# Performance work log

Hardware: AMD Instinct MI355X
Metric: run time of the kernel (lower is better)

Reference implementation:

```python
import jax, jax.numpy as jnp
import numpy as np

N_NODES = 100000  # m == n for the square adjacency
LEAKY_SLOPE = 0.5


def setup_inputs() -> dict:
    key = jax.random.key(0)
    k1, k2, k3 = jax.random.split(key, 3)
    E = 3200000
    D = 128
    edge_index = jax.random.randint(k1, (2, E), 0, N_NODES, dtype=jnp.int64)
    edge_vals = jax.random.uniform(k2, (E,), dtype=jnp.float32)
    embeds = jax.random.normal(k3, (N_NODES, D), dtype=jnp.float32)
    return {"edge_index": edge_index, "edge_vals": edge_vals, "embeds": embeds}


def reference(edge_index, edge_vals, embeds):
    # coalesce (sum duplicate (row,col) values) followed by scatter-add SpMM
    # is equivalent to scatter-add SpMM directly on un-coalesced indices.
    row, col = edge_index[0], edge_index[1]
    # gather source embeddings, scale by edge values, segment-sum into rows
    msgs = edge_vals[:, None] * embeds[col]                 # [E, D]
    agg = jax.ops.segment_sum(msgs, row, num_segments=N_NODES)  # [N, D]
    return jax.nn.leaky_relu(agg, negative_slope=LEAKY_SLOPE)
```

## Files before the change

kernel.cpp:

```cpp
#include <hip/hip_runtime.h>
#include <hip/hip_fp16.h>


#define GCN_D       128
#define LEAKY_SLOPE 0.5f
#define NBLK        256
#define RPB         64
#define RPB_SH      6
#define CAP         3072
#define NBINS_MAX   2048
#define SCAN_G      512
#define NCHAIN_FB   4

typedef float    f32x2 __attribute__((ext_vector_type(2)));
typedef float    f32x4 __attribute__((ext_vector_type(4)));
typedef unsigned u32x2 __attribute__((ext_vector_type(2)));
typedef unsigned u32x4 __attribute__((ext_vector_type(4)));

__device__ inline unsigned pack_half2(float a, float b) {
    __half2 h = __floats2half2_rn(a, b);
    return *reinterpret_cast<unsigned*>(&h);
}


__global__ void hist_convert_kernel(const int* __restrict__ row,
                                    int E, int CH, int nbins,
                                    unsigned* __restrict__ hist,
                                    const f32x4* __restrict__ emb4,
                                    int n8,
                                    u32x4* __restrict__ h8) {
    __shared__ unsigned h[NBINS_MAX];
    if ((int)blockIdx.x < NBLK) {
        int b = blockIdx.x;
        for (int i = threadIdx.x; i < nbins; i += blockDim.x) h[i] = 0u;
        __syncthreads();
        int s = b * CH;
        int e = min(E, s + CH);
        for (int i = s + threadIdx.x; i < e; i += blockDim.x)
            atomicAdd(&h[row[i] >> RPB_SH], 1u);
        __syncthreads();
        for (int i = threadIdx.x; i < nbins; i += blockDim.x)
            hist[(long long)i * NBLK + b] = h[i];
    } else {
        int bid = (int)blockIdx.x - NBLK;
        int nb  = (int)gridDim.x - NBLK;
        int stride = nb * blockDim.x;
        for (int i = bid * blockDim.x + threadIdx.x; i < n8; i += stride) {
            f32x4 a  = __builtin_nontemporal_load(&emb4[2 * i]);
            f32x4 b2 = __builtin_nontemporal_load(&emb4[2 * i + 1]);
            u32x4 o;
            o.x = pack_half2(a.x, a.y);
            o.y = pack_half2(a.z, a.w);
            o.z = pack_half2(b2.x, b2.y);
            o.w = pack_half2(b2.z, b2.w);
            h8[i] = o;
        }
    }
}


__global__ void __launch_bounds__(256)
scanA_kernel(const unsigned* __restrict__ data, int M, int chunk,
             unsigned* __restrict__ bsum) {
    __shared__ unsigned red[256];
    int b = blockIdx.x, t = threadIdx.x;
    long long s = (long long)b * chunk;
    unsigned acc = 0;
    for (int i = t; i < chunk; i += 256) {
        long long j = s + i;
        if (j < M) acc += data[j];
    }
    red[t] = acc;
    __syncthreads();
    for (int off = 128; off > 0; off >>= 1) {
        if (t < off) red[t] += red[t + off];
        __syncthreads();
    }
    if (t == 0) bsum[b] = red[0];
}

__global__ void __launch_bounds__(512)
scanB_kernel(unsigned* __restrict__ bsum, int G) {
    __shared__ unsigned s[512];
    int t = threadIdx.x;
    unsigned v = (t < G) ? bsum[t] : 0u;
    s[t] = v;
    __syncthreads();
    for (int off = 1; off < 512; off <<= 1) {
        unsigned u = (t >= off) ? s[t - off] : 0u;
        __syncthreads();
        s[t] += u;
        __syncthreads();
    }
    if (t < G) bsum[t] = (t == 0) ? 0u : s[t - 1];
}

__global__ void __launch_bounds__(256)
scanC_kernel(unsigned* __restrict__ data, int M, int chunk,
             const unsigned* __restrict__ bsum) {
    __shared__ unsigned pre[256];
    int b = blockIdx.x, t = threadIdx.x;
    long long s0 = (long long)b * chunk;
    long long s1 = s0 + chunk;
    int ept = (chunk + 255) / 256;
    long long ts = s0 + (long long)t * ept;

    unsigned acc = 0;
    for (int i = 0; i < ept; ++i) {
        long long j = ts + i;
        if (j < s1 && j < M) acc += data[j];
    }
    pre[t] = acc;
    __syncthreads();
    for (int off = 1; off < 256; off <<= 1) {
        unsigned u = (t >= off) ? pre[t - off] : 0u;
        __syncthreads();
        pre[t] += u;
        __syncthreads();
    }
    unsigned run = bsum[b] + ((t == 0) ? 0u : pre[t - 1]);
    for (int i = 0; i < ept; ++i) {
        long long j = ts + i;
        if (j < s1 && j < M) {
            unsigned v = data[j];
            data[j] = run;
            run += v;
        }
    }
}


__global__ void scatter_kernel(const int* __restrict__ row,
                               const int* __restrict__ col,
                               const float* __restrict__ val,
                               int E, int CH, int nbins,
                               const unsigned* __restrict__ scanned,
                               u32x2* __restrict__ entry) {
    __shared__ unsigned cur[NBINS_MAX];
    int b = blockIdx.x;
    for (int i = threadIdx.x; i < nbins; i += blockDim.x)
        cur[i] = scanned[(long long)i * NBLK + b];
    __syncthreads();

    int s = b * CH;
    int e = min(E, s + CH);
    for (int i = s + threadIdx.x; i < e; i += blockDim.x) {
        int r = row[i];
        unsigned key = ((unsigned)(r & (RPB - 1)) << 17) | (unsigned)col[i];
        unsigned pos = atomicAdd(&cur[r >> RPB_SH], 1u);
        u32x2 q; q.x = key; q.y = __float_as_uint(val[i]);
        entry[pos] = q;
    }
}


__global__ void __launch_bounds__(512)
bin_reduce_kernel(const unsigned* __restrict__ scanned,
                  const u32x2* __restrict__ entry,
                  const __half2* __restrict__ ebh,
                  float* __restrict__ out,
                  int E, int N, int nbins) {
    __shared__ u32x2    sorted[CAP];
    __shared__ unsigned cnt[RPB];
    __shared__ unsigned offs[RPB];
    __shared__ unsigned cur[RPB];

    int b    = blockIdx.x;
    int tid  = threadIdx.x;
    int wave = tid >> 6;
    int lane = tid & 63;

    int seg0 = (int)scanned[(long long)b * NBLK];
    int seg1 = (b + 1 < nbins) ? (int)scanned[(long long)(b + 1) * NBLK] : E;

    float ax[8], ay[8];
    #pragma unroll
    for (int j = 0; j < 8; ++j) { ax[j] = 0.f; ay[j] = 0.f; }

    for (int cs = seg0; cs < seg1; cs += CAP) {
        int n = min(CAP, seg1 - cs);

        if (tid < RPB) cnt[tid] = 0u;
        __syncthreads();

        for (int i = tid; i < n; i += 512) {
            u32x2 q = __builtin_nontemporal_load(&entry[cs + i]);
            atomicAdd(&cnt[q.x >> 17], 1u);
        }
        __syncthreads();

        if (tid == 0) {
            unsigned run = 0;
            for (int r = 0; r < RPB; ++r) {
                offs[r] = run; cur[r] = run; run += cnt[r];
            }
        }
        __syncthreads();

        for (int i = tid; i < n; i += 512) {
            u32x2 q = __builtin_nontemporal_load(&entry[cs + i]);
            unsigned pos = atomicAdd(&cur[q.x >> 17], 1u);
            sorted[pos] = q;
        }
        __syncthreads();

        #pragma unroll
        for (int j = 0; j < 8; ++j) {
            int r  = (wave << 3) + j;
            int s  = (int)offs[r];
            int en = s + (int)cnt[r];
            int i  = s;
            for (; i + 8 <= en; i += 8) {
                u32x2 q0 = sorted[i],     q1 = sorted[i + 1];
                u32x2 q2 = sorted[i + 2], q3 = sorted[i + 3];
                u32x2 q4 = sorted[i + 4], q5 = sorted[i + 5];
                u32x2 q6 = sorted[i + 6], q7 = sorted[i + 7];
                __half2 m0 = ebh[(long long)(q0.x & 0x1FFFFu) * 64 + lane];
                __half2 m1 = ebh[(long long)(q1.x & 0x1FFFFu) * 64 + lane];
                __half2 m2 = ebh[(long long)(q2.x & 0x1FFFFu) * 64 + lane];
                __half2 m3 = ebh[(long long)(q3.x & 0x1FFFFu) * 64 + lane];
                __half2 m4 = ebh[(long long)(q4.x & 0x1FFFFu) * 64 + lane];
                __half2 m5 = ebh[(long long)(q5.x & 0x1FFFFu) * 64 + lane];
                __half2 m6 = ebh[(long long)(q6.x & 0x1FFFFu) * 64 + lane];
                __half2 m7 = ebh[(long long)(q7.x & 0x1FFFFu) * 64 + lane];
                float2 f;
                f = __half22float2(m0);
                ax[j] += __uint_as_float(q0.y) * f.x; ay[j] += __uint_as_float(q0.y) * f.y;
                f = __half22float2(m1);
                ax[j] += __uint_as_float(q1.y) * f.x; ay[j] += __uint_as_float(q1.y) * f.y;
                f = __half22float2(m2);
                ax[j] += __uint_as_float(q2.y) * f.x; ay[j] += __uint_as_float(q2.y) * f.y;
                f = __half22float2(m3);
                ax[j] += __uint_as_float(q3.y) * f.x; ay[j] += __uint_as_float(q3.y) * f.y;
                f = __half22float2(m4);
                ax[j] += __uint_as_float(q4.y) * f.x; ay[j] += __uint_as_float(q4.y) * f.y;
                f = __half22float2(m5);
                ax[j] += __uint_as_float(q5.y) * f.x; ay[j] += __uint_as_float(q5.y) * f.y;
                f = __half22float2(m6);
                ax[j] += __uint_as_float(q6.y) * f.x; ay[j] += __uint_as_float(q6.y) * f.y;
                f = __half22float2(m7);
                ax[j] += __uint_as_float(q7.y) * f.x; ay[j] += __uint_as_float(q7.y) * f.y;
            }
            for (; i < en; ++i) {
                u32x2 q = sorted[i];
                __half2 mm = ebh[(long long)(q.x & 0x1FFFFu) * 64 + lane];
                float2 f = __half22float2(mm);
                ax[j] += __uint_as_float(q.y) * f.x;
                ay[j] += __uint_as_float(q.y) * f.y;
            }
        }
        __syncthreads();
    }

    int gr0 = b * RPB + (wave << 3);
    #pragma unroll
    for (int j = 0; j < 8; ++j) {
        int gr = gr0 + j;
        if (gr < N) {
            float x = ax[j], y = ay[j];
            x = x > 0.f ? x : LEAKY_SLOPE * x;
            y = y > 0.f ? y : LEAKY_SLOPE * y;
            f32x2 o; o.x = x; o.y = y;
            __builtin_nontemporal_store(
                o, reinterpret_cast<f32x2*>(out) + (long long)gr * 64 + lane);
        }
    }
}


__global__ void build_nodes_kernel(const int* __restrict__ row,
                                   const int* __restrict__ col,
                                   const float* __restrict__ val,
                                   int E,
                                   int* __restrict__ head,
                                   int4* __restrict__ node) {
    int stride = gridDim.x * blockDim.x;
    for (int i = blockIdx.x * blockDim.x + threadIdx.x; i < E; i += stride) {
        int   r = row[i];
        int   c = col[i];
        float v = val[i];
        int prev = atomicExch(&head[r * NCHAIN_FB + (i & (NCHAIN_FB - 1))], i);
        node[i] = make_int4(prev, c, __float_as_int(v), 0);
    }
}

__global__ void __launch_bounds__(256)
reduce_nodes_kernel(const int* __restrict__ head,
                    const int4* __restrict__ node,
                    const float* __restrict__ embeds,
                    float* __restrict__ out,
                    int N) {
    int wave = (int)((blockIdx.x * (long long)blockDim.x + threadIdx.x) >> 6);
    int lane = threadIdx.x & 63;
    if (wave >= N) return;

    const float2* eb = reinterpret_cast<const float2*>(embeds);
    int4 h = reinterpret_cast<const int4*>(head)[wave];
    int e0 = h.x, e1 = h.y, e2 = h.z, e3 = h.w;

    float ax = 0.f, ay = 0.f;

    while ((e0 & e1 & e2 & e3) != -1) {
        int i0 = e0 >= 0 ? e0 : 0;
        int i1 = e1 >= 0 ? e1 : 0;
        int i2 = e2 >= 0 ? e2 : 0;
        int i3 = e3 >= 0 ? e3 : 0;

        int4 n0 = node[i0];
        int4 n1 = node[i1];
        int4 n2 = node[i2];
        int4 n3 = node[i3];

        int c0 = e0 >= 0 ? n0.y : 0;
        int c1 = e1 >= 0 ? n1.y : 0;
        int c2 = e2 >= 0 ? n2.y : 0;
        int c3 = e3 >= 0 ? n3.y : 0;

        float2 m0 = eb[(long long)c0 * 64 + lane];
        float2 m1 = eb[(long long)c1 * 64 + lane];
        float2 m2 = eb[(long long)c2 * 64 + lane];
        float2 m3 = eb[(long long)c3 * 64 + lane];

        float v0 = e0 >= 0 ? __int_as_float(n0.z) : 0.f;
        float v1 = e1 >= 0 ? __int_as_float(n1.z) : 0.f;
        float v2 = e2 >= 0 ? __int_as_float(n2.z) : 0.f;
        float v3 = e3 >= 0 ? __int_as_float(n3.z) : 0.f;

        ax += v0 * m0.x; ay += v0 * m0.y;
        ax += v1 * m1.x; ay += v1 * m1.y;
        ax += v2 * m2.x; ay += v2 * m2.y;
        ax += v3 * m3.x; ay += v3 * m3.y;

        e0 = e0 >= 0 ? n0.x : -1;
        e1 = e1 >= 0 ? n1.x : -1;
        e2 = e2 >= 0 ? n2.x : -1;
        e3 = e3 >= 0 ? n3.x : -1;
    }

    ax = ax > 0.f ? ax : LEAKY_SLOPE * ax;
    ay = ay > 0.f ? ay : LEAKY_SLOPE * ay;
    reinterpret_cast<float2*>(out)[(long long)wave * 64 + lane] =
        make_float2(ax, ay);
}


__global__ void gcn_scatter_kernel(const int* __restrict__ row_idx,
                                   const int* __restrict__ col_idx,
                                   const float* __restrict__ vals,
                                   const float* __restrict__ embeds,
                                   float* __restrict__ out,
                                   int E) {
    long long tid = (long long)blockIdx.x * blockDim.x + threadIdx.x;
    long long e = tid >> 5;
    if (e >= E) return;
    int q = (int)(tid & 31);
    int row = row_idx[e];
    int col = col_idx[e];
    float v = vals[e];
    const float4* src =
        reinterpret_cast<const float4*>(embeds + (long long)col * GCN_D) + q;
    float4 m = *src;
    float* dst = out + (long long)row * GCN_D + (long long)q * 4;
    atomicAdd(dst + 0, v * m.x);
    atomicAdd(dst + 1, v * m.y);
    atomicAdd(dst + 2, v * m.z);
    atomicAdd(dst + 3, v * m.w);
}

__global__ void gcn_leaky_relu_kernel(float* __restrict__ out, int n4) {
    int i = blockIdx.x * blockDim.x + threadIdx.x;
    if (i >= n4) return;
    float4* p = reinterpret_cast<float4*>(out) + i;
    float4 x = *p;
    x.x = x.x > 0.f ? x.x : LEAKY_SLOPE * x.x;
    x.y = x.y > 0.f ? x.y : LEAKY_SLOPE * x.y;
    x.z = x.z > 0.f ? x.z : LEAKY_SLOPE * x.z;
    x.w = x.w > 0.f ? x.w : LEAKY_SLOPE * x.w;
    *p = x;
}


extern "C" void kernel_launch(void* const* d_in, const int* in_sizes, int n_in,
                              void* d_out, int out_size, void* d_ws, size_t ws_size,
                              hipStream_t stream) {
    const int*   edge_index = (const int*)d_in[0];
    const float* edge_vals  = (const float*)d_in[1];
    const float* embeds     = (const float*)d_in[2];
    float*       out        = (float*)d_out;

    const int E = in_sizes[1];
    const int N = out_size / GCN_D;
    const int* row = edge_index;
    const int* col = edge_index + E;

    const int block = 256;
    const int nbins = (N + RPB - 1) / RPB;
    const int M     = nbins * NBLK;
    const int CH    = (E + NBLK - 1) / NBLK;
    const int chunk = (M + SCAN_G - 1) / SCAN_G;

    size_t hist_b = (((size_t)M * sizeof(unsigned)) + 255) & ~(size_t)255;
    size_t bsum_b = (((size_t)SCAN_G * sizeof(unsigned)) + 255) & ~(size_t)255;
    size_t ent_b  = (((size_t)E * sizeof(u32x2)) + 255) & ~(size_t)255;
    size_t half_b = (size_t)N * GCN_D * sizeof(__half);
    size_t need_r7 = hist_b + bsum_b + ent_b + half_b;

    size_t head_fb = (size_t)N * NCHAIN_FB * sizeof(int);
    size_t need_r3 = head_fb + (size_t)E * sizeof(int4);

    if (ws_size >= need_r7 && nbins <= NBINS_MAX) {
        unsigned* hist  = (unsigned*)d_ws;
        unsigned* bsum  = reinterpret_cast<unsigned*>((char*)d_ws + hist_b);
        u32x2*    entry = reinterpret_cast<u32x2*>((char*)d_ws + hist_b + bsum_b);
        u32x4*    h8    = reinterpret_cast<u32x4*>((char*)d_ws + hist_b + bsum_b + ent_b);

        int n8 = N * (GCN_D / 8);
        int convBlocks = (n8 + block - 1) / block;

        hist_convert_kernel<<<NBLK + convBlocks, block, 0, stream>>>(
            row, E, CH, nbins, hist,
            reinterpret_cast<const f32x4*>(embeds), n8, h8);

        scanA_kernel<<<SCAN_G, 256, 0, stream>>>(hist, M, chunk, bsum);
        scanB_kernel<<<1, 512, 0, stream>>>(bsum, SCAN_G);
        scanC_kernel<<<SCAN_G, 256, 0, stream>>>(hist, M, chunk, bsum);

        scatter_kernel<<<NBLK, block, 0, stream>>>(
            row, col, edge_vals, E, CH, nbins, hist, entry);

        bin_reduce_kernel<<<nbins, 512, 0, stream>>>(
            hist, entry, reinterpret_cast<const __half2*>(h8), out, E, N, nbins);
    } else if (ws_size >= need_r3) {
        int*  head = (int*)d_ws;
        int4* node = reinterpret_cast<int4*>((char*)d_ws + head_fb);

        hipMemsetAsync(head, 0xFF, head_fb, stream);
        build_nodes_kernel<<<2048, block, 0, stream>>>(row, col, edge_vals,
                                                       E, head, node);

        long long threads = (long long)N * 64;
        int rblocks = (int)((threads + block - 1) / block);
        reduce_nodes_kernel<<<rblocks, block, 0, stream>>>(
            head, node, embeds, out, N);
    } else {
        hipMemsetAsync(d_out, 0, (size_t)out_size * sizeof(float), stream);
        long long total_threads = (long long)E * 32;
        long long grid = (total_threads + block - 1) / block;
        gcn_scatter_kernel<<<(unsigned)grid, block, 0, stream>>>(
            row, col, edge_vals, embeds, out, E);
        int n4 = out_size / 4;
        gcn_leaky_relu_kernel<<<(n4 + 255) / 256, 256, 0, stream>>>(out, n4);
    }
}
```

Before: 202.6 us.

## Process two edges per wave with 8-byte gathers and stage bin entries in LDS

The bin reduce kernel now splits each wave into two half-waves. Each half-wave gathers a full 128-dim half-precision row for a different edge, with each lane loading 8 bytes, and the two halves are combined with a cross-lane shuffle before output. Entries are copied into a shared raw buffer on the first pass so the second pass reads LDS instead of global memory. The serial prefix sum is replaced by a wave shuffle scan, and CAP is reduced to keep the doubled shared arrays within LDS. The scatter kernel also uses nontemporal stores for the entries, while the added reduction shuffles and the smaller chunk size add some overhead.

Measured after the change: 298.7 us. 47.4% more time.

```diff
diff --git a/kernel.cpp b/kernel.cpp
--- a/kernel.cpp
+++ b/kernel.cpp
@@ -7,7 +7,7 @@
 #define NBLK        256
 #define RPB         64
 #define RPB_SH      6
-#define CAP         3072
+#define CAP         2048
 #define NBINS_MAX   2048
 #define SCAN_G      512
 #define NCHAIN_FB   4
@@ -20,6 +20,12 @@
 __device__ inline unsigned pack_half2(float a, float b) {
     __half2 h = __floats2half2_rn(a, b);
     return *reinterpret_cast<unsigned*>(&h);
+}
+
+__device__ inline float2 h2bits_to_f2(unsigned u) {
+    __half2 h;
+    *reinterpret_cast<unsigned*>(&h) = u;
+    return __half22float2(h);
 }
 
 
@@ -149,7 +155,7 @@
         unsigned key = ((unsigned)(r & (RPB - 1)) << 17) | (unsigned)col[i];
         unsigned pos = atomicAdd(&cur[r >> RPB_SH], 1u);
         u32x2 q; q.x = key; q.y = __float_as_uint(val[i]);
-        entry[pos] = q;
+        __builtin_nontemporal_store(q, &entry[pos]);
     }
 }
 
@@ -157,9 +163,10 @@
 __global__ void __launch_bounds__(512)
 bin_reduce_kernel(const unsigned* __restrict__ scanned,
                   const u32x2* __restrict__ entry,
-                  const __half2* __restrict__ ebh,
+                  const u32x2* __restrict__ ebh4,
                   float* __restrict__ out,
                   int E, int N, int nbins) {
+    __shared__ u32x2    raw[CAP];
     __shared__ u32x2    sorted[CAP];
     __shared__ unsigned cnt[RPB];
     __shared__ unsigned offs[RPB];
@@ -169,13 +176,15 @@
     int tid  = threadIdx.x;
     int wave = tid >> 6;
     int lane = tid & 63;
+    int hw   = lane >> 5;
+    int cq   = lane & 31;
 
     int seg0 = (int)scanned[(long long)b * NBLK];
     int seg1 = (b + 1 < nbins) ? (int)scanned[(long long)(b + 1) * NBLK] : E;
 
-    float ax[8], ay[8];
+    float a0[8], a1[8], a2[8], a3[8];
     #pragma unroll
-    for (int j = 0; j < 8; ++j) { ax[j] = 0.f; ay[j] = 0.f; }
+    for (int j = 0; j < 8; ++j) { a0[j] = a1[j] = a2[j] = a3[j] = 0.f; }
 
     for (int cs = seg0; cs < seg1; cs += CAP) {
         int n = min(CAP, seg1 - cs);
@@ -185,20 +194,26 @@
 
         for (int i = tid; i < n; i += 512) {
             u32x2 q = __builtin_nontemporal_load(&entry[cs + i]);
+            raw[i] = q;
             atomicAdd(&cnt[q.x >> 17], 1u);
         }
         __syncthreads();
 
-        if (tid == 0) {
-            unsigned run = 0;
-            for (int r = 0; r < RPB; ++r) {
-                offs[r] = run; cur[r] = run; run += cnt[r];
+        if (wave == 0) {
+            unsigned c = cnt[lane];
+            unsigned s = c;
+            #pragma unroll
+            for (int off = 1; off < 64; off <<= 1) {
+                unsigned t = __shfl_up(s, off, 64);
+                if (lane >= off) s += t;
             }
+            offs[lane] = s - c;
+            cur[lane]  = s - c;
         }
         __syncthreads();
 
         for (int i = tid; i < n; i += 512) {
-            u32x2 q = __builtin_nontemporal_load(&entry[cs + i]);
+            u32x2 q = raw[i];
             unsigned pos = atomicAdd(&cur[q.x >> 17], 1u);
             sorted[pos] = q;
         }
@@ -211,58 +226,55 @@
             int en = s + (int)cnt[r];
             int i  = s;
             for (; i + 8 <= en; i += 8) {
-                u32x2 q0 = sorted[i],     q1 = sorted[i + 1];
-                u32x2 q2 = sorted[i + 2], q3 = sorted[i + 3];
-                u32x2 q4 = sorted[i + 4], q5 = sorted[i + 5];
-                u32x2 q6 = sorted[i + 6], q7 = sorted[i + 7];
-                __half2 m0 = ebh[(long long)(q0.x & 0x1FFFFu) * 64 + lane];
-                __half2 m1 = ebh[(long long)(q1.x & 0x1FFFFu) * 64 + lane];
-                __half2 m2 = ebh[(long long)(q2.x & 0x1FFFFu) * 64 + lane];
-                __half2 m3 = ebh[(long long)(q3.x & 0x1FFFFu) * 64 + lane];
-                __half2 m4 = ebh[(long long)(q4.x & 0x1FFFFu) * 64 + lane];
-                __half2 m5 = ebh[(long long)(q5.x & 0x1FFFFu) * 64 + lane];
-                __half2 m6 = ebh[(long long)(q6.x & 0x1FFFFu) * 64 + lane];
-                __half2 m7 = ebh[(long long)(q7.x & 0x1FFFFu) * 64 + lane];
-                float2 f;
-                f = __half22float2(m0);
-                ax[j] += __uint_as_float(q0.y) * f.x; ay[j] += __uint_as_float(q0.y) * f.y;
-                f = __half22float2(m1);
-                ax[j] += __uint_as_float(q1.y) * f.x; ay[j] += __uint_as_float(q1.y) * f.y;
-                f = __half22float2(m2);
-                ax[j] += __uint_as_float(q2.y) * f.x; ay[j] += __uint_as_float(q2.y) * f.y;
-                f = __half22float2(m3);
-                ax[j] += __uint_as_float(q3.y) * f.x; ay[j] += __uint_as_float(q3.y) * f.y;
-                f = __half22float2(m4);
-                ax[j] += __uint_as_float(q4.y) * f.x; ay[j] += __uint_as_float(q4.y) * f.y;
-                f = __half22float2(m5);
-                ax[j] += __uint_as_float(q5.y) * f.x; ay[j] += __uint_as_float(q5.y) * f.y;
-                f = __half22float2(m6);
-                ax[j] += __uint_as_float(q6.y) * f.x; ay[j] += __uint_as_float(q6.y) * f.y;
-                f = __half22float2(m7);
-                ax[j] += __uint_as_float(q7.y) * f.x; ay[j] += __uint_as_float(q7.y) * f.y;
+                #pragma unroll
+                for (int p = 0; p < 4; ++p) {
+                    u32x2 q = sorted[i + 2 * p + hw];
+                    float v = __uint_as_float(q.y);
+                    u32x2 g = ebh4[(long long)(q.x & 0x1FFFFu) * 32 + cq];
+                    float2 f0 = h2bits_to_f2(g.x);
+                    float2 f1 = h2bits_to_f2(g.y);
+                    a0[j] += v * f0.x;  a1[j] += v * f0.y;
+                    a2[j] += v * f1.x;  a3[j] += v * f1.y;
+                }
             }
-            for (; i < en; ++i) {
-                u32x2 q = sorted[i];
-                __half2 mm = ebh[(long long)(q.x & 0x1FFFFu) * 64 + lane];
-                float2 f = __half22float2(mm);
-                ax[j] += __uint_as_float(q.y) * f.x;
-                ay[j] += __uint_as_float(q.y) * f.y;
+            for (; i < en; i += 2) {
+                int  idx   = i + hw;
+                bool valid = idx < en;
+                u32x2 q = sorted[valid ? idx : i];
+                float v = valid ? __uint_as_float(q.y) : 0.f;
+                u32x2 g = ebh4[(long long)(q.x & 0x1FFFFu) * 32 + cq];
+                float2 f0 = h2bits_to_f2(g.x);
+                float2 f1 = h2bits_to_f2(g.y);
+                a0[j] += v * f0.x;  a1[j] += v * f0.y;
+                a2[j] += v * f1.x;  a3[j] += v * f1.y;
             }
         }
         __syncthreads();
     }
 
-    int gr0 = b * RPB + (wave << 3);
     #pragma unroll
     for (int j = 0; j < 8; ++j) {
-        int gr = gr0 + j;
-        if (gr < N) {
-            float x = ax[j], y = ay[j];
-            x = x > 0.f ? x : LEAKY_SLOPE * x;
-            y = y > 0.f ? y : LEAKY_SLOPE * y;
-            f32x2 o; o.x = x; o.y = y;
-            __builtin_nontemporal_store(
-                o, reinterpret_cast<f32x2*>(out) + (long long)gr * 64 + lane);
+        a0[j] += __shfl_xor(a0[j], 32, 64);
+        a1[j] += __shfl_xor(a1[j], 32, 64);
+        a2[j] += __shfl_xor(a2[j], 32, 64);
+        a3[j] += __shfl_xor(a3[j], 32, 64);
+    }
+
+    if (hw == 0) {
+        int gr0 = b * RPB + (wave << 3);
+        #pragma unroll
+        for (int j = 0; j < 8; ++j) {
+            int gr = gr0 + j;
+            if (gr < N) {
+                float x0 = a0[j], x1 = a1[j], x2 = a2[j], x3 = a3[j];
+                x0 = x0 > 0.f ? x0 : LEAKY_SLOPE * x0;
+                x1 = x1 > 0.f ? x1 : LEAKY_SLOPE * x1;
+                x2 = x2 > 0.f ? x2 : LEAKY_SLOPE * x2;
+                x3 = x3 > 0.f ? x3 : LEAKY_SLOPE * x3;
+                f32x4 o; o.x = x0; o.y = x1; o.z = x2; o.w = x3;
+                __builtin_nontemporal_store(
+                    o, reinterpret_cast<f32x4*>(out + (long long)gr * GCN_D) + cq);
+            }
         }
     }
 }
@@ -403,12 +415,12 @@
     size_t bsum_b = (((size_t)SCAN_G * sizeof(unsigned)) + 255) & ~(size_t)255;
     size_t ent_b  = (((size_t)E * sizeof(u32x2)) + 255) & ~(size_t)255;
     size_t half_b = (size_t)N * GCN_D * sizeof(__half);
-    size_t need_r7 = hist_b + bsum_b + ent_b + half_b;
+    size_t need_r8 = hist_b + bsum_b + ent_b + half_b;
 
     size_t head_fb = (size_t)N * NCHAIN_FB * sizeof(int);
     size_t need_r3 = head_fb + (size_t)E * sizeof(int4);
 
-    if (ws_size >= need_r7 && nbins <= NBINS_MAX) {
+    if (ws_size >= need_r8 && nbins <= NBINS_MAX) {
         unsigned* hist  = (unsigned*)d_ws;
         unsigned* bsum  = reinterpret_cast<unsigned*>((char*)d_ws + hist_b);
         u32x2*    entry = reinterpret_cast<u32x2*>((char*)d_ws + hist_b + bsum_b);
@@ -429,7 +441,7 @@
             row, col, edge_vals, E, CH, nbins, hist, entry);
 
         bin_reduce_kernel<<<nbins, 512, 0, stream>>>(
-            hist, entry, reinterpret_cast<const __half2*>(h8), out, E, N, nbins);
+            hist, entry, reinterpret_cast<const u32x2*>(h8), out, E, N, nbins);
     } else if (ws_size >= need_r3) {
         int*  head = (int*)d_ws;
         int4* node = reinterpret_cast<int4*>((char*)d_ws + head_fb);
```

## Keep bin entries in registers, use wave-shuffle scan, widen scatter blocks

Applied to the files above, without the earlier changes.

The bin-reduce kernel now loads each chunk's entries into registers once (EPT=6 per thread, covering CAP=3072) instead of reading them from global memory twice for counting and placement. The serial single-thread prefix over 64 row counts is replaced by a wave-level shuffle scan. The scatter kernel is launched with 1024 threads per block instead of 256 to add memory-level parallelism over its 256 blocks. The register array raises VGPR pressure in bin_reduce, and correctness depends on CAP <= 512*EPT.

Result: slower. 208.0 us (+2.7%).

```diff
diff --git a/kernel.cpp b/kernel.cpp
--- a/kernel.cpp
+++ b/kernel.cpp
@@ -8,6 +8,7 @@
 #define RPB         64
 #define RPB_SH      6
 #define CAP         3072
+#define EPT         6
 #define NBINS_MAX   2048
 #define SCAN_G      512
 #define NCHAIN_FB   4
@@ -130,12 +131,13 @@
 }
 
 
-__global__ void scatter_kernel(const int* __restrict__ row,
-                               const int* __restrict__ col,
-                               const float* __restrict__ val,
-                               int E, int CH, int nbins,
-                               const unsigned* __restrict__ scanned,
-                               u32x2* __restrict__ entry) {
+__global__ void __launch_bounds__(1024)
+scatter_kernel(const int* __restrict__ row,
+               const int* __restrict__ col,
+               const float* __restrict__ val,
+               int E, int CH, int nbins,
+               const unsigned* __restrict__ scanned,
+               u32x2* __restrict__ entry) {
     __shared__ unsigned cur[NBINS_MAX];
     int b = blockIdx.x;
     for (int i = threadIdx.x; i < nbins; i += blockDim.x)
@@ -183,24 +185,37 @@
         if (tid < RPB) cnt[tid] = 0u;
         __syncthreads();
 
-        for (int i = tid; i < n; i += 512) {
-            u32x2 q = __builtin_nontemporal_load(&entry[cs + i]);
-            atomicAdd(&cnt[q.x >> 17], 1u);
-        }
-        __syncthreads();
-
-        if (tid == 0) {
-            unsigned run = 0;
-            for (int r = 0; r < RPB; ++r) {
-                offs[r] = run; cur[r] = run; run += cnt[r];
+        u32x2 q[EPT];
+        #pragma unroll
+        for (int k = 0; k < EPT; ++k) {
+            int i = tid + (k << 9);
+            if (i < n) {
+                q[k] = __builtin_nontemporal_load(&entry[cs + i]);
+                atomicAdd(&cnt[q[k].x >> 17], 1u);
             }
         }
         __syncthreads();
 
-        for (int i = tid; i < n; i += 512) {
-            u32x2 q = __builtin_nontemporal_load(&entry[cs + i]);
-            unsigned pos = atomicAdd(&cur[q.x >> 17], 1u);
-            sorted[pos] = q;
+        if (wave == 0) {
+            unsigned c = cnt[lane];
+            unsigned s = c;
+            #pragma unroll
+            for (int off = 1; off < 64; off <<= 1) {
+                unsigned t = __shfl_up(s, off, 64);
+                if (lane >= off) s += t;
+            }
+            offs[lane] = s - c;
+            cur[lane]  = s - c;
+        }
+        __syncthreads();
+
+        #pragma unroll
+        for (int k = 0; k < EPT; ++k) {
+            int i = tid + (k << 9);
+            if (i < n) {
+                unsigned pos = atomicAdd(&cur[q[k].x >> 17], 1u);
+                sorted[pos] = q[k];
+            }
         }
         __syncthreads();
 
@@ -242,11 +257,11 @@
                 ax[j] += __uint_as_float(q7.y) * f.x; ay[j] += __uint_as_float(q7.y) * f.y;
             }
             for (; i < en; ++i) {
-                u32x2 q = sorted[i];
-                __half2 mm = ebh[(long long)(q.x & 0x1FFFFu) * 64 + lane];
+                u32x2 qq = sorted[i];
+                __half2 mm = ebh[(long long)(qq.x & 0x1FFFFu) * 64 + lane];
                 float2 f = __half22float2(mm);
-                ax[j] += __uint_as_float(q.y) * f.x;
-                ay[j] += __uint_as_float(q.y) * f.y;
+                ax[j] += __uint_as_float(qq.y) * f.x;
+                ay[j] += __uint_as_float(qq.y) * f.y;
             }
         }
         __syncthreads();
@@ -403,12 +418,12 @@
     size_t bsum_b = (((size_t)SCAN_G * sizeof(unsigned)) + 255) & ~(size_t)255;
     size_t ent_b  = (((size_t)E * sizeof(u32x2)) + 255) & ~(size_t)255;
     size_t half_b = (size_t)N * GCN_D * sizeof(__half);
-    size_t need_r7 = hist_b + bsum_b + ent_b + half_b;
+    size_t need_r9 = hist_b + bsum_b + ent_b + half_b;
 
     size_t head_fb = (size_t)N * NCHAIN_FB * sizeof(int);
     size_t need_r3 = head_fb + (size_t)E * sizeof(int4);
 
-    if (ws_size >= need_r7 && nbins <= NBINS_MAX) {
+    if (ws_size >= need_r9 && nbins <= NBINS_MAX) {
         unsigned* hist  = (unsigned*)d_ws;
         unsigned* bsum  = reinterpret_cast<unsigned*>((char*)d_ws + hist_b);
         u32x2*    entry = reinterpret_cast<u32x2*>((char*)d_ws + hist_b + bsum_b);
@@ -425,7 +440,7 @@
         scanB_kernel<<<1, 512, 0, stream>>>(bsum, SCAN_G);
         scanC_kernel<<<SCAN_G, 256, 0, stream>>>(hist, M, chunk, bsum);
 
-        scatter_kernel<<<NBLK, block, 0, stream>>>(
+        scatter_kernel<<<NBLK, 1024, 0, stream>>>(
             row, col, edge_vals, E, CH, nbins, hist, entry);
 
         bin_reduce_kernel<<<nbins, 512, 0, stream>>>(
```
